# Performance work log

Measured on AMD Instinct MI355X. Metric: run time of the kernel, lower is better.

The kernel has to match this reference:

```python
import jax, jax.numpy as jnp
import numpy as np

D_MODEL, N_HEADS, D_K, BASE, EPS = 1024, 16, 64, 10000, 1e-6
SCALE = 1.0 / np.sqrt(D_K)


def rope(x):
    # x: [b, s, h, d]
    b, s, h, d = x.shape
    d2 = d // 2
    theta = 1.0 / (BASE ** (jnp.arange(0, d, 2, dtype=jnp.float32) / d))  # [d2]
    idx_theta = jnp.arange(s, dtype=jnp.float32)[:, None] * theta[None, :]  # [s, d2]
    idx_theta2 = jnp.concatenate([idx_theta, idx_theta], axis=1)  # [s, d]
    cos = jnp.cos(idx_theta2)[None, :, None, :]
    sin = jnp.sin(idx_theta2)[None, :, None, :]
    neg_half = jnp.concatenate([-x[..., d2:], x[..., :d2]], axis=-1)
    return x * cos + neg_half * sin


def setup_inputs() -> dict:
    key = jax.random.key(0)
    ks = jax.random.split(key, 10)
    B, S = 2, 2048
    std = 1.0 / np.sqrt(D_MODEL)
    return {
        "h": jax.random.normal(ks[0], (B, S, D_MODEL), dtype=jnp.float32),
        "wq": jax.random.normal(ks[1], (D_MODEL, N_HEADS * D_K), dtype=jnp.float32) * std,
        "bq": jnp.zeros((N_HEADS * D_K,), dtype=jnp.float32),
        "wk": jax.random.normal(ks[2], (D_MODEL, N_HEADS * D_K), dtype=jnp.float32) * std,
        "bk": jnp.zeros((N_HEADS * D_K,), dtype=jnp.float32),
        "wv": jax.random.normal(ks[3], (D_MODEL, N_HEADS * D_K), dtype=jnp.float32) * std,
        "bv": jnp.zeros((N_HEADS * D_K,), dtype=jnp.float32),
        "wo": jax.random.normal(ks[4], (N_HEADS * D_K, D_MODEL), dtype=jnp.float32) * std,
        "bo": jnp.zeros((D_MODEL,), dtype=jnp.float32),
        "g": jnp.ones((D_MODEL,), dtype=jnp.float32),
    }


def reference(h, wq, bq, wk, bk, wv, bv, wo, bo, g):
    B, S, _ = h.shape
    h_res = h
    # RMSNorm
    hn = h * jax.lax.rsqrt(jnp.mean(h * h, axis=-1, keepdims=True) + EPS) * g
    mh = (B, S, N_HEADS, D_K)
    q = (hn @ wq + bq).reshape(mh)
    k = (hn @ wk + bk).reshape(mh)
    v = (hn @ wv + bv).reshape(mh)
    q, k = rope(q), rope(k)
    attn = jnp.einsum('bihd,bjhd->bhij', q, k) * SCALE
    mask = jnp.tril(jnp.ones((S, S), dtype=bool))
    attn = jnp.where(mask, attn, -jnp.inf)
    attn = jax.nn.softmax(attn, axis=-1)
    out = jnp.einsum('bhij,bjhd->bihd', attn, v).reshape(B, S, N_HEADS * D_K)
    return out @ wo + bo + h_res
```

## Files before the change

kernel.cpp:

```cpp
#include <hip/hip_runtime.h>
#include <hip/hip_bf16.h>

#define D_MODEL 1024
#define NH 16
#define DK 64
#define SEQ 2048
#define BATCH 2
#define NTOK (BATCH * SEQ)
#define EPS 1e-6f

typedef __attribute__((ext_vector_type(4))) float f32x4;
typedef __attribute__((ext_vector_type(16))) float f32x16;
typedef __attribute__((ext_vector_type(8))) short s16x8;
typedef unsigned int u32;
typedef __hip_bfloat16 bf16;

#define AS1 __attribute__((address_space(1)))
#define AS3 __attribute__((address_space(3)))

static __device__ __forceinline__ s16x8 ld8(const bf16* p) {
    return *reinterpret_cast<const s16x8*>(p);
}
static __device__ __forceinline__ float b2f(short s) {
    return __uint_as_float(((u32)(unsigned short)s) << 16);
}

static __device__ __forceinline__ u32 cvtpk(float lo, float hi) {
    u32 r;
    asm volatile("v_cvt_pk_bf16_f32 %0, %1, %2" : "=v"(r) : "v"(lo), "v"(hi));
    return r;
}
static __device__ __forceinline__ void swap32(u32& a, u32& b) {
    asm volatile("v_permlane32_swap_b32 %0, %1" : "+v"(a), "+v"(b));
}
static __device__ __forceinline__ float exp2f_fast(float x) {
    float r;
    asm("v_exp_f32 %0, %1" : "=v"(r) : "v"(x));
    return r;
}
static __device__ __forceinline__ void gld_lds16(const bf16* g, bf16* l) {
    __builtin_amdgcn_global_load_lds((const AS1 void*)g, (AS3 void*)l, 16, 0, 0);
}

union W4 { s16x8 v; u32 w[4]; };

#define LDSW(arr, row, kc) ld8(&arr[(row)][(((kc) ^ ((row) & 7)) << 3)])

__global__ __launch_bounds__(256) void k_tab(float2* __restrict__ tab) {
    const int idx = blockIdx.x * 256 + threadIdx.x;
    const int s = idx >> 5, i = idx & 31;
    const float theta = __expf(-(float)i * 0.28782313662425572f);
    float sn, cs;
    sincosf((float)s * theta, &sn, &cs);
    tab[idx] = make_float2(cs, sn);
}

__global__ __launch_bounds__(256) void k_rmsnorm(const float* __restrict__ h,
                                                 const float* __restrict__ g,
                                                 bf16* __restrict__ hn) {
    const int row = blockIdx.x;
    const int tid = threadIdx.x;
    const float4 x = reinterpret_cast<const float4*>(h + (size_t)row * D_MODEL)[tid];
    float ss = x.x * x.x + x.y * x.y + x.z * x.z + x.w * x.w;
#pragma unroll
    for (int off = 32; off; off >>= 1) ss += __shfl_xor(ss, off);
    __shared__ float red[4];
    if ((tid & 63) == 0) red[tid >> 6] = ss;
    __syncthreads();
    const float tot = red[0] + red[1] + red[2] + red[3];
    const float rs = rsqrtf(tot * (1.0f / D_MODEL) + EPS);
    const float4 gg = reinterpret_cast<const float4*>(g)[tid];
    bf16* o = hn + (size_t)row * D_MODEL + tid * 4;
    o[0] = __float2bfloat16(x.x * rs * gg.x);
    o[1] = __float2bfloat16(x.y * rs * gg.y);
    o[2] = __float2bfloat16(x.z * rs * gg.z);
    o[3] = __float2bfloat16(x.w * rs * gg.w);
}

__global__ __launch_bounds__(256) void k_packT4(const float* __restrict__ wq,
                                                const float* __restrict__ wk,
                                                const float* __restrict__ wv,
                                                const float* __restrict__ wo,
                                                bf16* __restrict__ dst) {
    __shared__ float t[32][33];
    const int kt = blockIdx.x * 32;
    const int nt = blockIdx.y * 32;
    const float* W = (blockIdx.y < 32) ? wq : (blockIdx.y < 64) ? wk
                   : (blockIdx.y < 96) ? wv : wo;
    const int nl = nt & (D_MODEL - 1);
    const int tx = threadIdx.x, ty = threadIdx.y;
#pragma unroll
    for (int i = 0; i < 4; i++)
        t[ty + 8 * i][tx] = W[(size_t)(kt + ty + 8 * i) * D_MODEL + nl + tx];
    __syncthreads();
#pragma unroll
    for (int i = 0; i < 4; i++)
        dst[(size_t)(nt + ty + 8 * i) * D_MODEL + kt + tx] = __float2bfloat16(t[tx][ty + 8 * i]);
}

__global__ __launch_bounds__(256) void k_gemm64_qkv(const bf16* __restrict__ A,
                                                    const bf16* __restrict__ Bt,
                                                    const float* __restrict__ bq,
                                                    const float* __restrict__ bk,
                                                    const float* __restrict__ bv,
                                                    const float2* __restrict__ tab,
                                                    bf16* __restrict__ qb,
                                                    bf16* __restrict__ kpk,
                                                    bf16* __restrict__ vpk) {
    __shared__ __align__(16) char smem[16384];
    bf16(*As)[64] = (bf16(*)[64])smem;
    bf16(*Bs)[64] = (bf16(*)[64])(smem + 8192);
    const int tid = threadIdx.x;
    const int w = tid >> 6, lane = tid & 63, l16 = lane & 15, lq = lane >> 4;
    const int wr = w >> 1, wc = w & 1;
    const int col0 = blockIdx.x * 64;
    const int row0 = blockIdx.y * 64;
    const int grow = lane >> 3;
    const int scol = (((lane & 7) ^ grow) << 3);
    f32x4 acc[2][2];
#pragma unroll
    for (int i = 0; i < 2; i++)
#pragma unroll
        for (int j = 0; j < 2; j++) acc[i][j] = f32x4{0, 0, 0, 0};

    for (int kt = 0; kt < D_MODEL; kt += 64) {
        gld_lds16(A + (size_t)(row0 + w * 16 + grow) * D_MODEL + kt + scol,      &As[w * 16][0]);
        gld_lds16(A + (size_t)(row0 + w * 16 + 8 + grow) * D_MODEL + kt + scol,  &As[w * 16 + 8][0]);
        gld_lds16(Bt + (size_t)(col0 + w * 16 + grow) * D_MODEL + kt + scol,     &Bs[w * 16][0]);
        gld_lds16(Bt + (size_t)(col0 + w * 16 + 8 + grow) * D_MODEL + kt + scol, &Bs[w * 16 + 8][0]);
        __syncthreads();
        s16x8 af[2][2], bfr[2][2];
#pragma unroll
        for (int mi = 0; mi < 2; mi++)
#pragma unroll
            for (int ks = 0; ks < 2; ks++)
                af[mi][ks] = LDSW(As, wr * 32 + mi * 16 + l16, ks * 4 + lq);
#pragma unroll
        for (int ni = 0; ni < 2; ni++)
#pragma unroll
            for (int ks = 0; ks < 2; ks++)
                bfr[ni][ks] = LDSW(Bs, wc * 32 + ni * 16 + l16, ks * 4 + lq);
        __builtin_amdgcn_s_setprio(1);
#pragma unroll
        for (int ks = 0; ks < 2; ks++)
#pragma unroll
            for (int mi = 0; mi < 2; mi++)
#pragma unroll
                for (int ni = 0; ni < 2; ni++)
                    acc[mi][ni] = __builtin_amdgcn_mfma_f32_16x16x32_bf16(af[mi][ks], bfr[ni][ks], acc[mi][ni], 0, 0, 0);
        __builtin_amdgcn_s_setprio(0);
        __syncthreads();
    }

    const int sect = col0 >> 10;
    const int b_ = row0 >> 11;
    const int head = (col0 & 1023) >> 6;
    if (sect == 2) {
        const int e0 = (lq & 1) * 4;
        const int tileL = (row0 & (SEQ - 1)) >> 6;
        bf16* dstH = vpk + ((size_t)(b_ * NH + head) << 17);
#pragma unroll
        for (int ni = 0; ni < 2; ni++) {
            const int dloc = wc * 32 + ni * 16 + l16;
            const float bs = bv[(col0 & 1023) + dloc];
#pragma unroll
            for (int mi = 0; mi < 2; mi++) {
                const int m = wr * 2 + mi;
                size_t off = ((((size_t)(tileL * 2 + (dloc >> 5)) * 4 + m) * 64
                               + ((lq >> 1) & 1) * 32 + (dloc & 31)) << 3) + e0;
                uint2 pv;
                pv.x = cvtpk(acc[mi][ni][0] + bs, acc[mi][ni][1] + bs);
                pv.y = cvtpk(acc[mi][ni][2] + bs, acc[mi][ni][3] + bs);
                *reinterpret_cast<uint2*>(dstH + off) = pv;
            }
        }
        return;
    }
    bf16(*Cs)[72] = (bf16(*)[72])smem;
    const float* bias = (sect == 0) ? bq : bk;
#pragma unroll
    for (int ni = 0; ni < 2; ni++) {
        const int cl = wc * 32 + ni * 16 + l16;
        const float bs = bias[(col0 & 1023) + cl];
#pragma unroll
        for (int mi = 0; mi < 2; mi++) {
            const int rl = wr * 32 + mi * 16 + lq * 4;
#pragma unroll
            for (int r = 0; r < 4; r++)
                Cs[rl + r][cl] = __float2bfloat16(acc[mi][ni][r] + bs);
        }
    }
    __syncthreads();
    const int row = tid >> 2, q = tid & 3;
    const int s_ = (row0 + row) & (SEQ - 1);
    const float2* tb = tab + s_ * 32 + q * 8;
    const float qs = (sect == 0) ? 0.18033688011112042f : 1.0f;
    const s16x8 vlo = ld8(&Cs[row][q * 8]);
    const s16x8 vhi = ld8(&Cs[row][q * 8 + 32]);
    u32 plo[4], phi[4];
#pragma unroll
    for (int e2 = 0; e2 < 4; e2++) {
        float a[2], b[2];
#pragma unroll
        for (int k = 0; k < 2; k++) {
            const int e = e2 * 2 + k;
            const float2 cs = tb[e];
            const float x1 = b2f(vlo[e]), x2 = b2f(vhi[e]);
            a[k] = (x1 * cs.x - x2 * cs.y) * qs;
            b[k] = (x2 * cs.x + x1 * cs.y) * qs;
        }
        plo[e2] = cvtpk(a[0], a[1]);
        phi[e2] = cvtpk(b[0], b[1]);
    }
    if (sect == 0) {
        bf16* qdst = qb + (((size_t)(b_ * NH + head) * SEQ + s_) << 6);
        *reinterpret_cast<uint4*>(qdst + q * 8)      = make_uint4(plo[0], plo[1], plo[2], plo[3]);
        *reinterpret_cast<uint4*>(qdst + 32 + q * 8) = make_uint4(phi[0], phi[1], phi[2], phi[3]);
    } else {
        bf16* kdst = kpk + ((size_t)(b_ * NH + head) << 17);
        const int jb = s_ >> 5, j31 = s_ & 31;
        const size_t offL = (((size_t)(jb * 4 + (q >> 1)) * 64 + (q & 1) * 32 + j31) << 3);
        const size_t offH = (((size_t)(jb * 4 + ((q + 4) >> 1)) * 64 + ((q + 4) & 1) * 32 + j31) << 3);
        *reinterpret_cast<uint4*>(kdst + offL) = make_uint4(plo[0], plo[1], plo[2], plo[3]);
        *reinterpret_cast<uint4*>(kdst + offH) = make_uint4(phi[0], phi[1], phi[2], phi[3]);
    }
}

__global__ __launch_bounds__(256) void k_attn4(const bf16* __restrict__ qg,
                                               const bf16* __restrict__ kp,
                                               const bf16* __restrict__ vp,
                                               bf16* __restrict__ ao) {
    const int tid = threadIdx.x;
    const int w = tid >> 6;
    const int lane = tid & 63;
    const int l31 = lane & 31;
    const int hi = lane >> 5;
    const int bid = blockIdx.x;
    const int blk = (bid >> 3) & 15;
    const int bh  = (bid & 7) + ((bid >> 7) << 3);
    int pos;
    switch (w) {
        case 0:  pos = blk;      break;
        case 1:  pos = 31 - blk; break;
        case 2:  pos = 32 + blk; break;
        default: pos = 63 - blk; break;
    }
    const int qw = pos << 5;
    const int qrow = qw + l31;

    const bf16* qptr = qg + (((size_t)bh * SEQ + qrow) << 6) + 8 * hi;
    s16x8 qf[4];
#pragma unroll
    for (int t = 0; t < 4; t++) qf[t] = ld8(qptr + 16 * t);

    f32x16 o0, o1;
#pragma unroll
    for (int r = 0; r < 16; r++) { o0[r] = 0.0f; o1[r] = 0.0f; }
    float m_run = -1e30f, l_run = 0.0f;

    const int nfull = qw >> 6;
    const int ntot  = (qw + 95) >> 6;
    const bf16* kbase = kp + ((size_t)bh << 17);
    const bf16* vbase = vp + ((size_t)bh << 17);

    s16x8 kA[8], kB[8], vC[8];
#pragma unroll
    for (int t = 0; t < 8; t++) kA[t] = ld8(kbase + (((size_t)t * 64 + lane) << 3));

    auto att_step = [&](s16x8(&KC)[8], s16x8(&KN)[8], const int kt) {
        const int kb = kt << 6;
#pragma unroll
        for (int t = 0; t < 8; t++)
            vC[t] = ld8(vbase + (((size_t)(kt * 8 + t) * 64 + lane) << 3));
        f32x16 s0, s1;
#pragma unroll
        for (int r = 0; r < 16; r++) { s0[r] = 0.0f; s1[r] = 0.0f; }
        __builtin_amdgcn_s_setprio(1);
#pragma unroll
        for (int t = 0; t < 4; t++) {
            s0 = __builtin_amdgcn_mfma_f32_32x32x16_bf16(KC[t],     qf[t], s0, 0, 0, 0);
            s1 = __builtin_amdgcn_mfma_f32_32x32x16_bf16(KC[4 + t], qf[t], s1, 0, 0, 0);
        }
        __builtin_amdgcn_s_setprio(0);
        const int ktn = (kt + 1 < ntot) ? kt + 1 : kt;
#pragma unroll
        for (int t = 0; t < 8; t++)
            KN[t] = ld8(kbase + (((size_t)(ktn * 8 + t) * 64 + lane) << 3));
        float p[32];
#pragma unroll
        for (int r = 0; r < 16; r++) { p[r] = s0[r]; p[16 + r] = s1[r]; }
        if (kt >= nfull) {
#pragma unroll
            for (int r = 0; r < 32; r++) {
                const int j = kb + 8 * (r >> 2) + (r & 3) + 4 * hi;
                if (j > qrow) p[r] = -3.0e38f;
            }
        }
        float m16[16];
#pragma unroll
        for (int r = 0; r < 16; r++) m16[r] = fmaxf(p[r], p[r + 16]);
#pragma unroll
        for (int r = 0; r < 8; r++) m16[r] = fmaxf(m16[r], m16[r + 8]);
#pragma unroll
        for (int r = 0; r < 4; r++) m16[r] = fmaxf(m16[r], m16[r + 4]);
        float mx = fmaxf(fmaxf(m16[0], m16[1]), fmaxf(m16[2], m16[3]));
        mx = fmaxf(mx, __shfl_xor(mx, 32));
        if (!__all(mx <= m_run + 8.0f)) {
            const float mn = fmaxf(m_run, mx);
            const float alpha = exp2f_fast(m_run - mn);
            m_run = mn;
            l_run *= alpha;
#pragma unroll
            for (int r = 0; r < 16; r++) { o0[r] *= alpha; o1[r] *= alpha; }
        }
        float s4[4] = {0, 0, 0, 0};
#pragma unroll
        for (int r = 0; r < 32; r++) { p[r] = exp2f_fast(p[r] - m_run); s4[r & 3] += p[r]; }
        float rs = (s4[0] + s4[1]) + (s4[2] + s4[3]);
        rs += __shfl_xor(rs, 32);
        l_run += rs;
        u32 pk_[16];
#pragma unroll
        for (int a = 0; a < 8; a++) {
            pk_[2 * a]     = cvtpk(p[4 * a],     p[4 * a + 1]);
            pk_[2 * a + 1] = cvtpk(p[4 * a + 2], p[4 * a + 3]);
        }
        __builtin_amdgcn_s_setprio(1);
#pragma unroll
        for (int m = 0; m < 4; m++) {
            u32 b0 = pk_[4 * m],     b2 = pk_[4 * m + 2];
            u32 b1 = pk_[4 * m + 1], b3 = pk_[4 * m + 3];
            swap32(b0, b2);
            swap32(b1, b3);
            W4 B; B.w[0] = b0; B.w[1] = b1; B.w[2] = b2; B.w[3] = b3;
            o0 = __builtin_amdgcn_mfma_f32_32x32x16_bf16(vC[m],     B.v, o0, 0, 0, 0);
            o1 = __builtin_amdgcn_mfma_f32_32x32x16_bf16(vC[4 + m], B.v, o1, 0, 0, 0);
        }
        __builtin_amdgcn_s_setprio(0);
    };

    int kt = 0;
    for (;;) {
        att_step(kA, kB, kt); if (++kt == ntot) break;
        att_step(kB, kA, kt); if (++kt == ntot) break;
    }

    const float inv = 1.0f / l_run;
    const int b_ = bh >> 4, h_ = bh & (NH - 1);
    bf16* orow = ao + (((size_t)(b_ * SEQ + qrow)) << 10) + (h_ << 6);
#pragma unroll
    for (int g = 0; g < 4; g++) {
        {
            uint2 val;
            val.x = cvtpk(o0[4 * g] * inv, o0[4 * g + 1] * inv);
            val.y = cvtpk(o0[4 * g + 2] * inv, o0[4 * g + 3] * inv);
            *reinterpret_cast<uint2*>(orow + 8 * g + 4 * hi) = val;
        }
        {
            uint2 val;
            val.x = cvtpk(o1[4 * g] * inv, o1[4 * g + 1] * inv);
            val.y = cvtpk(o1[4 * g + 2] * inv, o1[4 * g + 3] * inv);
            *reinterpret_cast<uint2*>(orow + 32 + 8 * g + 4 * hi) = val;
        }
    }
}

__global__ __launch_bounds__(256) void k_gemm64_out(const bf16* __restrict__ A,
                                                    const bf16* __restrict__ Bt,
                                                    const float* __restrict__ bo,
                                                    const float* __restrict__ hres,
                                                    float* __restrict__ out) {
    __shared__ __align__(16) char smem[16384];
    bf16(*As)[64] = (bf16(*)[64])smem;
    bf16(*Bs)[64] = (bf16(*)[64])(smem + 8192);
    const int tid = threadIdx.x;
    const int w = tid >> 6, lane = tid & 63, l16 = lane & 15, lq = lane >> 4;
    const int wr = w >> 1, wc = w & 1;
    const int col0 = blockIdx.x * 64;
    const int row0 = blockIdx.y * 64;
    const int grow = lane >> 3;
    const int scol = (((lane & 7) ^ grow) << 3);
    f32x4 acc[2][2];
#pragma unroll
    for (int i = 0; i < 2; i++)
#pragma unroll
        for (int j = 0; j < 2; j++) acc[i][j] = f32x4{0, 0, 0, 0};

    for (int kt = 0; kt < D_MODEL; kt += 64) {
        gld_lds16(A + (size_t)(row0 + w * 16 + grow) * D_MODEL + kt + scol,      &As[w * 16][0]);
        gld_lds16(A + (size_t)(row0 + w * 16 + 8 + grow) * D_MODEL + kt + scol,  &As[w * 16 + 8][0]);
        gld_lds16(Bt + (size_t)(col0 + w * 16 + grow) * D_MODEL + kt + scol,     &Bs[w * 16][0]);
        gld_lds16(Bt + (size_t)(col0 + w * 16 + 8 + grow) * D_MODEL + kt + scol, &Bs[w * 16 + 8][0]);
        __syncthreads();
        s16x8 af[2][2], bfr[2][2];
#pragma unroll
        for (int mi = 0; mi < 2; mi++)
#pragma unroll
            for (int ks = 0; ks < 2; ks++)
                af[mi][ks] = LDSW(As, wr * 32 + mi * 16 + l16, ks * 4 + lq);
#pragma unroll
        for (int ni = 0; ni < 2; ni++)
#pragma unroll
            for (int ks = 0; ks < 2; ks++)
                bfr[ni][ks] = LDSW(Bs, wc * 32 + ni * 16 + l16, ks * 4 + lq);
        __builtin_amdgcn_s_setprio(1);
#pragma unroll
        for (int ks = 0; ks < 2; ks++)
#pragma unroll
            for (int mi = 0; mi < 2; mi++)
#pragma unroll
                for (int ni = 0; ni < 2; ni++)
                    acc[mi][ni] = __builtin_amdgcn_mfma_f32_16x16x32_bf16(af[mi][ks], bfr[ni][ks], acc[mi][ni], 0, 0, 0);
        __builtin_amdgcn_s_setprio(0);
        __syncthreads();
    }
#pragma unroll
    for (int ni = 0; ni < 2; ni++) {
        const int col = col0 + wc * 32 + ni * 16 + l16;
        const float bs = bo[col];
#pragma unroll
        for (int mi = 0; mi < 2; mi++) {
#pragma unroll
            for (int r = 0; r < 4; r++) {
                const int row = row0 + wr * 32 + mi * 16 + lq * 4 + r;
                out[(size_t)row * D_MODEL + col] =
                    acc[mi][ni][r] + bs + hres[(size_t)row * D_MODEL + col];
            }
        }
    }
}

extern "C" void kernel_launch(void* const* d_in, const int* in_sizes, int n_in,
                              void* d_out, int out_size, void* d_ws, size_t ws_size,
                              hipStream_t stream) {
    (void)in_sizes; (void)n_in; (void)out_size; (void)ws_size;
    const float* h  = (const float*)d_in[0];
    const float* wq = (const float*)d_in[1];
    const float* bq = (const float*)d_in[2];
    const float* wk = (const float*)d_in[3];
    const float* bk = (const float*)d_in[4];
    const float* wv = (const float*)d_in[5];
    const float* bv = (const float*)d_in[6];
    const float* wo = (const float*)d_in[7];
    const float* bo = (const float*)d_in[8];
    const float* g  = (const float*)d_in[9];
    float* out = (float*)d_out;

    char* ws = (char*)d_ws;
    size_t off = 0;
    auto carve = [&](size_t bytes) {
        void* p = ws + off;
        off += (bytes + 255) & ~(size_t)255;
        return p;
    };
    bf16* hn    = (bf16*)carve((size_t)NTOK * D_MODEL * 2);
    bf16* wallT = (bf16*)carve((size_t)4 * D_MODEL * D_MODEL * 2);
    bf16* wqkvT = wallT;
    bf16* woT   = wallT + (size_t)3 * D_MODEL * D_MODEL;
    bf16* qb    = (bf16*)carve((size_t)BATCH * NH * SEQ * DK * 2);
    bf16* kpk   = (bf16*)carve((size_t)BATCH * NH * SEQ * DK * 2);
    bf16* vpk   = (bf16*)carve((size_t)BATCH * NH * SEQ * DK * 2);
    bf16* ao    = (bf16*)carve((size_t)NTOK * D_MODEL * 2);
    float2* tab = (float2*)carve((size_t)SEQ * 32 * sizeof(float2));

    k_tab<<<256, 256, 0, stream>>>(tab);
    k_rmsnorm<<<NTOK, 256, 0, stream>>>(h, g, hn);
    k_packT4<<<dim3(32, 128), dim3(32, 8), 0, stream>>>(wq, wk, wv, wo, wallT);
    k_gemm64_qkv<<<dim3(48, 64), 256, 0, stream>>>(hn, wqkvT, bq, bk, bv, tab, qb, kpk, vpk);
    k_attn4<<<512, 256, 0, stream>>>(qb, kpk, vpk, ao);
    k_gemm64_out<<<dim3(16, 64), 256, 0, stream>>>(ao, woT, bo, h, out);
}
```

Measured before the change: 120.8 us.

## Split attention KV range across wave pairs and fuse RoPE table into RMSNorm

The attention kernel now pairs waves on each 32-row query tile. Each wave in a pair processes half of the key tiles, and the two partial softmax states are merged through shared memory, flash-decoding style. The grid doubles to 1024 blocks and launch bounds request 4 blocks per CU, aiming for more parallelism and shorter per-wave serial chains. The RoPE sin/cos table generation moves into the RMSNorm kernel to drop one launch, at the cost of an LDS merge, a block barrier, and extra sincos work in the first 256 norm blocks.

After: 265.8 us. 120% more time.

```diff
diff --git a/kernel.cpp b/kernel.cpp
--- a/kernel.cpp
+++ b/kernel.cpp
@@ -46,18 +46,10 @@
 
 #define LDSW(arr, row, kc) ld8(&arr[(row)][(((kc) ^ ((row) & 7)) << 3)])
 
-__global__ __launch_bounds__(256) void k_tab(float2* __restrict__ tab) {
-    const int idx = blockIdx.x * 256 + threadIdx.x;
-    const int s = idx >> 5, i = idx & 31;
-    const float theta = __expf(-(float)i * 0.28782313662425572f);
-    float sn, cs;
-    sincosf((float)s * theta, &sn, &cs);
-    tab[idx] = make_float2(cs, sn);
-}
-
 __global__ __launch_bounds__(256) void k_rmsnorm(const float* __restrict__ h,
                                                  const float* __restrict__ g,
-                                                 bf16* __restrict__ hn) {
+                                                 bf16* __restrict__ hn,
+                                                 float2* __restrict__ tab) {
     const int row = blockIdx.x;
     const int tid = threadIdx.x;
     const float4 x = reinterpret_cast<const float4*>(h + (size_t)row * D_MODEL)[tid];
@@ -75,6 +67,14 @@
     o[1] = __float2bfloat16(x.y * rs * gg.y);
     o[2] = __float2bfloat16(x.z * rs * gg.z);
     o[3] = __float2bfloat16(x.w * rs * gg.w);
+    if (row < 256) {
+        const int idx = row * 256 + tid;
+        const int s = idx >> 5, i = idx & 31;
+        const float theta = __expf(-(float)i * 0.28782313662425572f);
+        float sn, cs;
+        sincosf((float)s * theta, &sn, &cs);
+        tab[idx] = make_float2(cs, sn);
+    }
 }
 
 __global__ __launch_bounds__(256) void k_packT4(const float* __restrict__ wq,
@@ -226,25 +226,22 @@
     }
 }
 
-__global__ __launch_bounds__(256) void k_attn4(const bf16* __restrict__ qg,
-                                               const bf16* __restrict__ kp,
-                                               const bf16* __restrict__ vp,
-                                               bf16* __restrict__ ao) {
+__global__ __launch_bounds__(256, 4) void k_attn5(const bf16* __restrict__ qg,
+                                                  const bf16* __restrict__ kp,
+                                                  const bf16* __restrict__ vp,
+                                                  bf16* __restrict__ ao) {
+    __shared__ float part[2][64][36];
     const int tid = threadIdx.x;
-    const int w = tid >> 6;
+    const int wid = tid >> 6;
     const int lane = tid & 63;
     const int l31 = lane & 31;
     const int hi = lane >> 5;
+    const int pi = wid >> 1;
+    const int h = wid & 1;
     const int bid = blockIdx.x;
-    const int blk = (bid >> 3) & 15;
-    const int bh  = (bid & 7) + ((bid >> 7) << 3);
-    int pos;
-    switch (w) {
-        case 0:  pos = blk;      break;
-        case 1:  pos = 31 - blk; break;
-        case 2:  pos = 32 + blk; break;
-        default: pos = 63 - blk; break;
-    }
+    const int blk = (bid >> 3) & 31;
+    const int bh  = (bid & 7) + ((bid >> 8) << 3);
+    const int pos = pi ? (63 - blk) : blk;
     const int qw = pos << 5;
     const int qrow = qw + l31;
 
@@ -260,12 +257,12 @@
 
     const int nfull = qw >> 6;
     const int ntot  = (qw + 95) >> 6;
+    const int kt0 = h ? (ntot >> 1) : 0;
+    const int kt1 = h ? ntot : (ntot >> 1);
     const bf16* kbase = kp + ((size_t)bh << 17);
     const bf16* vbase = vp + ((size_t)bh << 17);
 
     s16x8 kA[8], kB[8], vC[8];
-#pragma unroll
-    for (int t = 0; t < 8; t++) kA[t] = ld8(kbase + (((size_t)t * 64 + lane) << 3));
 
     auto att_step = [&](s16x8(&KC)[8], s16x8(&KN)[8], const int kt) {
         const int kb = kt << 6;
@@ -282,7 +279,7 @@
             s1 = __builtin_amdgcn_mfma_f32_32x32x16_bf16(KC[4 + t], qf[t], s1, 0, 0, 0);
         }
         __builtin_amdgcn_s_setprio(0);
-        const int ktn = (kt + 1 < ntot) ? kt + 1 : kt;
+        const int ktn = (kt + 1 < kt1) ? kt + 1 : kt;
 #pragma unroll
         for (int t = 0; t < 8; t++)
             KN[t] = ld8(kbase + (((size_t)(ktn * 8 + t) * 64 + lane) << 3));
@@ -339,27 +336,56 @@
         __builtin_amdgcn_s_setprio(0);
     };
 
-    int kt = 0;
-    for (;;) {
-        att_step(kA, kB, kt); if (++kt == ntot) break;
-        att_step(kB, kA, kt); if (++kt == ntot) break;
-    }
-
-    const float inv = 1.0f / l_run;
+    int kt = kt0;
+    if (kt < kt1) {
+#pragma unroll
+        for (int t = 0; t < 8; t++) kA[t] = ld8(kbase + (((size_t)(kt * 8 + t) * 64 + lane) << 3));
+        for (;;) {
+            att_step(kA, kB, kt); if (++kt == kt1) break;
+            att_step(kB, kA, kt); if (++kt == kt1) break;
+        }
+    }
+
+    if (h == 0) {
+        float* dst = &part[pi][lane][0];
+#pragma unroll
+        for (int r4 = 0; r4 < 4; r4++) {
+            *reinterpret_cast<float4*>(dst + r4 * 4) =
+                make_float4(o0[4 * r4], o0[4 * r4 + 1], o0[4 * r4 + 2], o0[4 * r4 + 3]);
+            *reinterpret_cast<float4*>(dst + 16 + r4 * 4) =
+                make_float4(o1[4 * r4], o1[4 * r4 + 1], o1[4 * r4 + 2], o1[4 * r4 + 3]);
+        }
+        dst[32] = m_run;
+        dst[33] = l_run;
+    }
+    __syncthreads();
+    if (h == 0) return;
+
+    const float* src = &part[pi][lane][0];
+    const float mA = src[32], lA = src[33];
+    const float mN = fmaxf(mA, m_run);
+    const float aA = exp2f_fast(mA - mN);
+    const float aB = exp2f_fast(m_run - mN);
+    const float inv = 1.0f / (lA * aA + l_run * aB);
+
     const int b_ = bh >> 4, h_ = bh & (NH - 1);
     bf16* orow = ao + (((size_t)(b_ * SEQ + qrow)) << 10) + (h_ << 6);
 #pragma unroll
     for (int g = 0; g < 4; g++) {
         {
             uint2 val;
-            val.x = cvtpk(o0[4 * g] * inv, o0[4 * g + 1] * inv);
-            val.y = cvtpk(o0[4 * g + 2] * inv, o0[4 * g + 3] * inv);
+            val.x = cvtpk((src[4 * g] * aA + o0[4 * g] * aB) * inv,
+                          (src[4 * g + 1] * aA + o0[4 * g + 1] * aB) * inv);
+            val.y = cvtpk((src[4 * g + 2] * aA + o0[4 * g + 2] * aB) * inv,
+                          (src[4 * g + 3] * aA + o0[4 * g + 3] * aB) * inv);
             *reinterpret_cast<uint2*>(orow + 8 * g + 4 * hi) = val;
         }
         {
             uint2 val;
-            val.x = cvtpk(o1[4 * g] * inv, o1[4 * g + 1] * inv);
-            val.y = cvtpk(o1[4 * g + 2] * inv, o1[4 * g + 3] * inv);
+            val.x = cvtpk((src[16 + 4 * g] * aA + o1[4 * g] * aB) * inv,
+                          (src[16 + 4 * g + 1] * aA + o1[4 * g + 1] * aB) * inv);
+            val.y = cvtpk((src[16 + 4 * g + 2] * aA + o1[4 * g + 2] * aB) * inv,
+                          (src[16 + 4 * g + 3] * aA + o1[4 * g + 3] * aB) * inv);
             *reinterpret_cast<uint2*>(orow + 32 + 8 * g + 4 * hi) = val;
         }
     }
@@ -463,10 +489,9 @@
     bf16* ao    = (bf16*)carve((size_t)NTOK * D_MODEL * 2);
     float2* tab = (float2*)carve((size_t)SEQ * 32 * sizeof(float2));
 
-    k_tab<<<256, 256, 0, stream>>>(tab);
-    k_rmsnorm<<<NTOK, 256, 0, stream>>>(h, g, hn);
+    k_rmsnorm<<<NTOK, 256, 0, stream>>>(h, g, hn, tab);
     k_packT4<<<dim3(32, 128), dim3(32, 8), 0, stream>>>(wq, wk, wv, wo, wallT);
     k_gemm64_qkv<<<dim3(48, 64), 256, 0, stream>>>(hn, wqkvT, bq, bk, bv, tab, qb, kpk, vpk);
-    k_attn4<<<512, 256, 0, stream>>>(qb, kpk, vpk, ao);
+    k_attn5<<<1024, 256, 0, stream>>>(qb, kpk, vpk, ao);
     k_gemm64_out<<<dim3(16, 64), 256, 0, stream>>>(ao, woT, bo, h, out);
 }
```

## Merge prep kernels and software-pipeline QK^T one tile ahead in attention

Applied to the files above, without the earlier changes.

Merges the RoPE table, RMSNorm and weight transpose/pack kernels into one launch so only one kernel is issued for setup work. In the attention kernel, the QK^T MFMAs for the next key tile now run before the softmax of the current tile, so matrix work can overlap the exp/max work. K loads are prefetched two tiles ahead. This holds more score accumulators live at once, which adds register pressure and may lower occupancy.

New measurement: 145.0 us. 20.0% more time.

```diff
diff --git a/kernel.cpp b/kernel.cpp
--- a/kernel.cpp
+++ b/kernel.cpp
@@ -46,56 +46,59 @@
 
 #define LDSW(arr, row, kc) ld8(&arr[(row)][(((kc) ^ ((row) & 7)) << 3)])
 
-__global__ __launch_bounds__(256) void k_tab(float2* __restrict__ tab) {
-    const int idx = blockIdx.x * 256 + threadIdx.x;
-    const int s = idx >> 5, i = idx & 31;
-    const float theta = __expf(-(float)i * 0.28782313662425572f);
-    float sn, cs;
-    sincosf((float)s * theta, &sn, &cs);
-    tab[idx] = make_float2(cs, sn);
-}
-
-__global__ __launch_bounds__(256) void k_rmsnorm(const float* __restrict__ h,
-                                                 const float* __restrict__ g,
-                                                 bf16* __restrict__ hn) {
-    const int row = blockIdx.x;
+__global__ __launch_bounds__(256) void k_prep(const float* __restrict__ h,
+                                              const float* __restrict__ g,
+                                              const float* __restrict__ wq,
+                                              const float* __restrict__ wk,
+                                              const float* __restrict__ wv,
+                                              const float* __restrict__ wo,
+                                              bf16* __restrict__ hn,
+                                              bf16* __restrict__ wallT,
+                                              float2* __restrict__ tab) {
+    const int bid = blockIdx.x;
     const int tid = threadIdx.x;
-    const float4 x = reinterpret_cast<const float4*>(h + (size_t)row * D_MODEL)[tid];
-    float ss = x.x * x.x + x.y * x.y + x.z * x.z + x.w * x.w;
-#pragma unroll
-    for (int off = 32; off; off >>= 1) ss += __shfl_xor(ss, off);
-    __shared__ float red[4];
-    if ((tid & 63) == 0) red[tid >> 6] = ss;
-    __syncthreads();
-    const float tot = red[0] + red[1] + red[2] + red[3];
-    const float rs = rsqrtf(tot * (1.0f / D_MODEL) + EPS);
-    const float4 gg = reinterpret_cast<const float4*>(g)[tid];
-    bf16* o = hn + (size_t)row * D_MODEL + tid * 4;
-    o[0] = __float2bfloat16(x.x * rs * gg.x);
-    o[1] = __float2bfloat16(x.y * rs * gg.y);
-    o[2] = __float2bfloat16(x.z * rs * gg.z);
-    o[3] = __float2bfloat16(x.w * rs * gg.w);
-}
-
-__global__ __launch_bounds__(256) void k_packT4(const float* __restrict__ wq,
-                                                const float* __restrict__ wk,
-                                                const float* __restrict__ wv,
-                                                const float* __restrict__ wo,
-                                                bf16* __restrict__ dst) {
-    __shared__ float t[32][33];
-    const int kt = blockIdx.x * 32;
-    const int nt = blockIdx.y * 32;
-    const float* W = (blockIdx.y < 32) ? wq : (blockIdx.y < 64) ? wk
-                   : (blockIdx.y < 96) ? wv : wo;
-    const int nl = nt & (D_MODEL - 1);
-    const int tx = threadIdx.x, ty = threadIdx.y;
-#pragma unroll
-    for (int i = 0; i < 4; i++)
-        t[ty + 8 * i][tx] = W[(size_t)(kt + ty + 8 * i) * D_MODEL + nl + tx];
-    __syncthreads();
-#pragma unroll
-    for (int i = 0; i < 4; i++)
-        dst[(size_t)(nt + ty + 8 * i) * D_MODEL + kt + tx] = __float2bfloat16(t[tx][ty + 8 * i]);
+    if (bid < 4096) {
+        const int row = bid;
+        const float4 x = reinterpret_cast<const float4*>(h + (size_t)row * D_MODEL)[tid];
+        float ss = x.x * x.x + x.y * x.y + x.z * x.z + x.w * x.w;
+#pragma unroll
+        for (int off = 32; off; off >>= 1) ss += __shfl_xor(ss, off);
+        __shared__ float red[4];
+        if ((tid & 63) == 0) red[tid >> 6] = ss;
+        __syncthreads();
+        const float tot = red[0] + red[1] + red[2] + red[3];
+        const float rs = rsqrtf(tot * (1.0f / D_MODEL) + EPS);
+        const float4 gg = reinterpret_cast<const float4*>(g)[tid];
+        bf16* o = hn + (size_t)row * D_MODEL + tid * 4;
+        o[0] = __float2bfloat16(x.x * rs * gg.x);
+        o[1] = __float2bfloat16(x.y * rs * gg.y);
+        o[2] = __float2bfloat16(x.z * rs * gg.z);
+        o[3] = __float2bfloat16(x.w * rs * gg.w);
+        if (row < 256) {
+            const int idx = row * 256 + tid;
+            const int s = idx >> 5, i = idx & 31;
+            const float theta = __expf(-(float)i * 0.28782313662425572f);
+            float sn, cs;
+            sincosf((float)s * theta, &sn, &cs);
+            tab[idx] = make_float2(cs, sn);
+        }
+    } else {
+        __shared__ float t[32][33];
+        const int bid2 = bid - 4096;
+        const int kt = (bid2 & 31) * 32;
+        const int by = bid2 >> 5;
+        const int nt = by * 32;
+        const float* W = (by < 32) ? wq : (by < 64) ? wk : (by < 96) ? wv : wo;
+        const int nl = nt & (D_MODEL - 1);
+        const int tx = tid & 31, ty = tid >> 5;
+#pragma unroll
+        for (int i = 0; i < 4; i++)
+            t[ty + 8 * i][tx] = W[(size_t)(kt + ty + 8 * i) * D_MODEL + nl + tx];
+        __syncthreads();
+#pragma unroll
+        for (int i = 0; i < 4; i++)
+            wallT[(size_t)(nt + ty + 8 * i) * D_MODEL + kt + tx] = __float2bfloat16(t[tx][ty + 8 * i]);
+    }
 }
 
 __global__ __launch_bounds__(256) void k_gemm64_qkv(const bf16* __restrict__ A,
@@ -226,7 +229,7 @@
     }
 }
 
-__global__ __launch_bounds__(256) void k_attn4(const bf16* __restrict__ qg,
+__global__ __launch_bounds__(256) void k_attn6(const bf16* __restrict__ qg,
                                                const bf16* __restrict__ kp,
                                                const bf16* __restrict__ vp,
                                                bf16* __restrict__ ao) {
@@ -264,41 +267,55 @@
     const bf16* vbase = vp + ((size_t)bh << 17);
 
     s16x8 kA[8], kB[8], vC[8];
+    f32x16 sA0, sA1, sB0, sB1;
+
 #pragma unroll
     for (int t = 0; t < 8; t++) kA[t] = ld8(kbase + (((size_t)t * 64 + lane) << 3));
-
-    auto att_step = [&](s16x8(&KC)[8], s16x8(&KN)[8], const int kt) {
-        const int kb = kt << 6;
+#pragma unroll
+    for (int r = 0; r < 16; r++) { sA0[r] = 0.0f; sA1[r] = 0.0f; }
+#pragma unroll
+    for (int t = 0; t < 4; t++) {
+        sA0 = __builtin_amdgcn_mfma_f32_32x32x16_bf16(kA[t],     qf[t], sA0, 0, 0, 0);
+        sA1 = __builtin_amdgcn_mfma_f32_32x32x16_bf16(kA[4 + t], qf[t], sA1, 0, 0, 0);
+    }
+    {
+        const int kn = (1 < ntot) ? 1 : 0;
+#pragma unroll
+        for (int t = 0; t < 8; t++) kB[t] = ld8(kbase + (((size_t)(kn * 8 + t) * 64 + lane) << 3));
+    }
+
+    auto process = [&](f32x16& c0, f32x16& c1, f32x16& n0, f32x16& n1,
+                       s16x8(&KN)[8], s16x8(&KP)[8], const int kt) {
 #pragma unroll
         for (int t = 0; t < 8; t++)
             vC[t] = ld8(vbase + (((size_t)(kt * 8 + t) * 64 + lane) << 3));
-        f32x16 s0, s1;
-#pragma unroll
-        for (int r = 0; r < 16; r++) { s0[r] = 0.0f; s1[r] = 0.0f; }
-        __builtin_amdgcn_s_setprio(1);
-#pragma unroll
-        for (int t = 0; t < 4; t++) {
-            s0 = __builtin_amdgcn_mfma_f32_32x32x16_bf16(KC[t],     qf[t], s0, 0, 0, 0);
-            s1 = __builtin_amdgcn_mfma_f32_32x32x16_bf16(KC[4 + t], qf[t], s1, 0, 0, 0);
-        }
-        __builtin_amdgcn_s_setprio(0);
-        const int ktn = (kt + 1 < ntot) ? kt + 1 : kt;
-#pragma unroll
-        for (int t = 0; t < 8; t++)
-            KN[t] = ld8(kbase + (((size_t)(ktn * 8 + t) * 64 + lane) << 3));
-        float p[32];
-#pragma unroll
-        for (int r = 0; r < 16; r++) { p[r] = s0[r]; p[16 + r] = s1[r]; }
+        if (kt + 1 < ntot) {
+#pragma unroll
+            for (int r = 0; r < 16; r++) { n0[r] = 0.0f; n1[r] = 0.0f; }
+            __builtin_amdgcn_s_setprio(1);
+#pragma unroll
+            for (int t = 0; t < 4; t++) {
+                n0 = __builtin_amdgcn_mfma_f32_32x32x16_bf16(KN[t],     qf[t], n0, 0, 0, 0);
+                n1 = __builtin_amdgcn_mfma_f32_32x32x16_bf16(KN[4 + t], qf[t], n1, 0, 0, 0);
+            }
+            __builtin_amdgcn_s_setprio(0);
+            const int kn2 = (kt + 2 < ntot) ? kt + 2 : kt + 1;
+#pragma unroll
+            for (int t = 0; t < 8; t++)
+                KP[t] = ld8(kbase + (((size_t)(kn2 * 8 + t) * 64 + lane) << 3));
+        }
+        const int kb = kt << 6;
         if (kt >= nfull) {
 #pragma unroll
-            for (int r = 0; r < 32; r++) {
-                const int j = kb + 8 * (r >> 2) + (r & 3) + 4 * hi;
-                if (j > qrow) p[r] = -3.0e38f;
+            for (int r = 0; r < 16; r++) {
+                const int j0 = kb + 8 * (r >> 2) + (r & 3) + 4 * hi;
+                if (j0 > qrow) c0[r] = -3.0e38f;
+                if (j0 + 32 > qrow) c1[r] = -3.0e38f;
             }
         }
         float m16[16];
 #pragma unroll
-        for (int r = 0; r < 16; r++) m16[r] = fmaxf(p[r], p[r + 16]);
+        for (int r = 0; r < 16; r++) m16[r] = fmaxf(c0[r], c1[r]);
 #pragma unroll
         for (int r = 0; r < 8; r++) m16[r] = fmaxf(m16[r], m16[r + 8]);
 #pragma unroll
@@ -315,15 +332,19 @@
         }
         float s4[4] = {0, 0, 0, 0};
 #pragma unroll
-        for (int r = 0; r < 32; r++) { p[r] = exp2f_fast(p[r] - m_run); s4[r & 3] += p[r]; }
+        for (int r = 0; r < 16; r++) { c0[r] = exp2f_fast(c0[r] - m_run); s4[r & 3] += c0[r]; }
+#pragma unroll
+        for (int r = 0; r < 16; r++) { c1[r] = exp2f_fast(c1[r] - m_run); s4[r & 3] += c1[r]; }
         float rs = (s4[0] + s4[1]) + (s4[2] + s4[3]);
         rs += __shfl_xor(rs, 32);
         l_run += rs;
         u32 pk_[16];
 #pragma unroll
-        for (int a = 0; a < 8; a++) {
-            pk_[2 * a]     = cvtpk(p[4 * a],     p[4 * a + 1]);
-            pk_[2 * a + 1] = cvtpk(p[4 * a + 2], p[4 * a + 3]);
+        for (int a = 0; a < 4; a++) {
+            pk_[2 * a]     = cvtpk(c0[4 * a],     c0[4 * a + 1]);
+            pk_[2 * a + 1] = cvtpk(c0[4 * a + 2], c0[4 * a + 3]);
+            pk_[2 * a + 8] = cvtpk(c1[4 * a],     c1[4 * a + 1]);
+            pk_[2 * a + 9] = cvtpk(c1[4 * a + 2], c1[4 * a + 3]);
         }
         __builtin_amdgcn_s_setprio(1);
 #pragma unroll
@@ -341,8 +362,8 @@
 
     int kt = 0;
     for (;;) {
-        att_step(kA, kB, kt); if (++kt == ntot) break;
-        att_step(kB, kA, kt); if (++kt == ntot) break;
+        process(sA0, sA1, sB0, sB1, kB, kA, kt); if (++kt == ntot) break;
+        process(sB0, sB1, sA0, sA1, kA, kB, kt); if (++kt == ntot) break;
     }
 
     const float inv = 1.0f / l_run;
@@ -463,10 +484,8 @@
     bf16* ao    = (bf16*)carve((size_t)NTOK * D_MODEL * 2);
     float2* tab = (float2*)carve((size_t)SEQ * 32 * sizeof(float2));
 
-    k_tab<<<256, 256, 0, stream>>>(tab);
-    k_rmsnorm<<<NTOK, 256, 0, stream>>>(h, g, hn);
-    k_packT4<<<dim3(32, 128), dim3(32, 8), 0, stream>>>(wq, wk, wv, wo, wallT);
+    k_prep<<<8192, 256, 0, stream>>>(h, g, wq, wk, wv, wo, hn, wallT, tab);
     k_gemm64_qkv<<<dim3(48, 64), 256, 0, stream>>>(hn, wqkvT, bq, bk, bv, tab, qb, kpk, vpk);
-    k_attn4<<<512, 256, 0, stream>>>(qb, kpk, vpk, ao);
+    k_attn6<<<512, 256, 0, stream>>>(qb, kpk, vpk, ao);
     k_gemm64_out<<<dim3(16, 64), 256, 0, stream>>>(ao, woT, bo, h, out);
 }
```
